# Kernel optimization log

Hardware: AMD Instinct MI355X
Metric: run time of the kernel (lower is better)

The kernel has to match this reference:

```python
import jax, jax.numpy as jnp
import numpy as np

N, H, W = 2048, 128, 128
SH_C0 = 0.28209479177387814
SH_C1 = 0.4886025119029199
_C2 = [1.0925484305920792, -1.0925484305920792, 0.31539156525252005, -1.0925484305920792, 0.5462742152960396]
_C3 = [-0.5900435899266435, 2.890611442640554, -0.4570457994644658, 0.3731763325901154, -0.4570457994644658, 1.445305721320277, -0.5900435899266435]


def _quat_to_rot(q):
    # q: [N,4] unit quaternions (w, x, y, z)
    w, x, y, z = q[:, 0], q[:, 1], q[:, 2], q[:, 3]
    R = jnp.stack([
        1 - 2 * (y * y + z * z), 2 * (x * y - w * z), 2 * (x * z + w * y),
        2 * (x * y + w * z), 1 - 2 * (x * x + z * z), 2 * (y * z - w * x),
        2 * (x * z - w * y), 2 * (y * z + w * x), 1 - 2 * (x * x + y * y)], axis=-1)
    return R.reshape(-1, 3, 3)


def _sh_to_color(sh, dirs):
    # sh: [N,16,3] degree-3 SH coeffs per channel; dirs: [N,3] unit view dirs
    x, y, z = dirs[:, 0:1], dirs[:, 1:2], dirs[:, 2:3]
    xx, yy, zz = x * x, y * y, z * z
    xy, yz, xz = x * y, y * z, x * z
    c = SH_C0 * sh[:, 0]
    c = c - SH_C1 * y * sh[:, 1] + SH_C1 * z * sh[:, 2] - SH_C1 * x * sh[:, 3]
    c = (c + _C2[0] * xy * sh[:, 4] + _C2[1] * yz * sh[:, 5]
         + _C2[2] * (2 * zz - xx - yy) * sh[:, 6] + _C2[3] * xz * sh[:, 7]
         + _C2[4] * (xx - yy) * sh[:, 8])
    c = (c + _C3[0] * y * (3 * xx - yy) * sh[:, 9] + _C3[1] * xy * z * sh[:, 10]
         + _C3[2] * y * (4 * zz - xx - yy) * sh[:, 11]
         + _C3[3] * z * (2 * zz - 3 * xx - 3 * yy) * sh[:, 12]
         + _C3[4] * x * (4 * zz - xx - yy) * sh[:, 13]
         + _C3[5] * z * (xx - yy) * sh[:, 14]
         + _C3[6] * x * (xx - 3 * yy) * sh[:, 15])
    return jnp.maximum(c + 0.5, 0.0)


def _forward(pws, shs, alphas_raw, scales_raw, rots_raw, Rcw, tcw, fx, fy, cx, cy, width, height):
    fx = jnp.float32(fx); fy = jnp.float32(fy)
    cx = jnp.float32(cx); cy = jnp.float32(cy)
    # GSModel activations
    alphas = jax.nn.sigmoid(alphas_raw)[:, 0]                    # [N]
    scales = jnp.exp(scales_raw)                                 # [N,3]
    rots = rots_raw / jnp.linalg.norm(rots_raw, axis=-1, keepdims=True)

    # --- project ---
    pcs = pws @ Rcw.T + tcw                                      # [N,3] camera coords
    depths = pcs[:, 2]
    valid = depths > 0.2                                         # frustum (near-plane) cull
    z = jnp.where(valid, depths, 1.0)
    u = jnp.stack([fx * pcs[:, 0] / z + cx, fy * pcs[:, 1] / z + cy], -1)  # [N,2]

    # --- cov3d = R S S^T R^T ---
    R = _quat_to_rot(rots)
    M = R * scales[:, None, :]                                   # R @ diag(s)
    cov3d = M @ jnp.swapaxes(M, 1, 2)                            # [N,3,3]

    # --- cov2d = T cov3d T^T + lowpass (T = J Rcw, EWA splatting) ---
    limx = 1.3 * 0.5 * width / fx
    limy = 1.3 * 0.5 * height / fy
    tx = jnp.clip(pcs[:, 0] / z, -limx, limx) * z
    ty = jnp.clip(pcs[:, 1] / z, -limy, limy) * z
    zero = jnp.zeros_like(z)
    J = jnp.stack([
        jnp.stack([fx / z, zero, -fx * tx / (z * z)], -1),
        jnp.stack([zero, fy / z, -fy * ty / (z * z)], -1)], 1)   # [N,2,3]
    T = J @ Rcw
    cov2d = T @ cov3d @ jnp.swapaxes(T, 1, 2) + 0.3 * jnp.eye(2, dtype=pws.dtype)

    # --- SH -> color ---
    twc = -Rcw.T @ tcw                                           # camera center in world
    d = pws - twc
    dirs = d / jnp.linalg.norm(d, axis=-1, keepdims=True)
    colors = _sh_to_color(shs.reshape(-1, 16, 3), dirs)          # [N,3]

    # --- inverse cov2d + 3-sigma screen extent (areas) ---
    a, b, c = cov2d[:, 0, 0], cov2d[:, 0, 1], cov2d[:, 1, 1]
    det = a * c - b * b
    valid = valid & (det > 0)
    det_s = jnp.where(valid, det, 1.0)
    cinv = jnp.stack([c / det_s, -b / det_s, a / det_s], -1)     # [N,3] = (c00, c01, c11)
    mid = 0.5 * (a + c)
    disc = jnp.sqrt(jnp.maximum(mid * mid - det, 0.1))
    areas = 3.0 * jnp.sqrt(jnp.maximum(jnp.stack([mid + disc, mid - disc], -1), 0.0))
    areas = jnp.where(valid[:, None], areas, 0.0)                # [N,2]

    # --- depth-sorted alpha compositing (dense reference for tile splat) ---
    order = jnp.argsort(depths)
    u_s, cinv_s = u[order], cinv[order]
    a_s, col_s, v_s = alphas[order], colors[order], valid[order]

    px = jnp.arange(width, dtype=pws.dtype) + 0.5
    py = jnp.arange(height, dtype=pws.dtype) + 0.5
    dx = px[None, None, :] - u_s[:, 0, None, None]               # [N,1,W]
    dy = py[None, :, None] - u_s[:, 1, None, None]               # [N,H,1]
    power = (-0.5 * (cinv_s[:, 0, None, None] * dx * dx
                     + cinv_s[:, 2, None, None] * dy * dy)
             - cinv_s[:, 1, None, None] * dx * dy)               # [N,H,W]
    g = jnp.minimum(a_s[:, None, None] * jnp.exp(jnp.minimum(power, 0.0)), 0.99)
    g = jnp.where((power <= 0.0) & (g >= 1.0 / 255.0) & v_s[:, None, None], g, 0.0)

    tau = jnp.cumprod(1.0 - g, axis=0)                           # transmittance
    T_excl = jnp.concatenate([jnp.ones_like(tau[:1]), tau[:-1]], axis=0)
    image = jnp.einsum('nhw,nc->chw', T_excl * g, col_s)         # [3,H,W]
    return image, areas


def setup_inputs() -> dict:
    key = jax.random.key(0)
    ks = jax.random.split(key, 6)
    pws = jax.random.normal(ks[0], (N, 3), dtype=jnp.float32) * jnp.array([2.0, 2.0, 1.0], jnp.float32)
    pws = pws.at[:, 2].add(5.0)  # in front of camera
    shs = jax.random.normal(ks[1], (N, 48), dtype=jnp.float32) * 0.5
    alphas_raw = jax.random.normal(ks[2], (N, 1), dtype=jnp.float32)
    scales_raw = jax.random.normal(ks[3], (N, 3), dtype=jnp.float32) * 0.3 - 2.0
    rots_raw = jax.random.normal(ks[4], (N, 4), dtype=jnp.float32)
    us = jnp.zeros((N, 2), dtype=jnp.float32)
    Rcw = jnp.eye(3, dtype=jnp.float32)
    tcw = jnp.zeros(3, dtype=jnp.float32)
    return dict(pws=pws, shs=shs, alphas_raw=alphas_raw, scales_raw=scales_raw,
                rots_raw=rots_raw, us=us, Rcw=Rcw, tcw=tcw,
                fx=400, fy=400, cx=64, cy=64, width=W, height=H)


def reference(pws, shs, alphas_raw, scales_raw, rots_raw, us, Rcw, tcw, fx, fy, cx, cy, width, height):
    # 'us' is accepted but recomputed inside (matches gsc.project overwriting it)
    return _forward(pws, shs, alphas_raw, scales_raw, rots_raw, Rcw, tcw, fx, fy, cx, cy, width, height)
```

## Files before the change

kernel.cpp:

```cpp
#include <hip/hip_runtime.h>
#include <hip/hip_fp16.h>
#include <math.h>

#define N_G   2048
#define IMG_W 128
#define IMG_H 128
#define NPIX (IMG_W * IMG_H)

#define RWAVES 16
#define RSUB   (N_G / RWAVES)

union f2h2 { float f; __half2 h; };

__global__ __launch_bounds__(64) void preprocess_k(
    const float* __restrict__ pws, const float* __restrict__ shs,
    const float* __restrict__ alphas_raw, const float* __restrict__ scales_raw,
    const float* __restrict__ rots_raw, const float* __restrict__ Rcw,
    const float* __restrict__ tcw,
    const int* __restrict__ fxp, const int* __restrict__ fyp,
    const int* __restrict__ cxp, const int* __restrict__ cyp,
    float* __restrict__ areas, float* __restrict__ depths,
    float* __restrict__ packed)
{
    int i = blockIdx.x * 64 + threadIdx.x;
    if (i >= N_G) return;

    const float fx = (float)fxp[0], fy = (float)fyp[0];
    const float cx = (float)cxp[0], cy = (float)cyp[0];
    const float R00 = Rcw[0], R01 = Rcw[1], R02 = Rcw[2];
    const float R10 = Rcw[3], R11 = Rcw[4], R12 = Rcw[5];
    const float R20 = Rcw[6], R21 = Rcw[7], R22 = Rcw[8];
    const float t0 = tcw[0], t1 = tcw[1], t2 = tcw[2];

    const float pwx = pws[i * 3 + 0], pwy = pws[i * 3 + 1], pwz = pws[i * 3 + 2];

    const float pcx = R00 * pwx + R01 * pwy + R02 * pwz + t0;
    const float pcy = R10 * pwx + R11 * pwy + R12 * pwz + t1;
    const float pcz = R20 * pwx + R21 * pwy + R22 * pwz + t2;

    const float depth = pcz;
    bool valid = depth > 0.2f;
    const float z = valid ? depth : 1.0f;

    const float ux = fx * pcx / z + cx;
    const float uy = fy * pcy / z + cy;

    const float4 q4 = ((const float4*)rots_raw)[i];
    float qw = q4.x, qx = q4.y, qy = q4.z, qz = q4.w;
    const float qn = sqrtf(qw * qw + qx * qx + qy * qy + qz * qz);
    qw /= qn; qx /= qn; qy /= qn; qz /= qn;
    float Rr[3][3];
    Rr[0][0] = 1.f - 2.f * (qy * qy + qz * qz);
    Rr[0][1] = 2.f * (qx * qy - qw * qz);
    Rr[0][2] = 2.f * (qx * qz + qw * qy);
    Rr[1][0] = 2.f * (qx * qy + qw * qz);
    Rr[1][1] = 1.f - 2.f * (qx * qx + qz * qz);
    Rr[1][2] = 2.f * (qy * qz - qw * qx);
    Rr[2][0] = 2.f * (qx * qz - qw * qy);
    Rr[2][1] = 2.f * (qy * qz + qw * qx);
    Rr[2][2] = 1.f - 2.f * (qx * qx + qy * qy);

    const float s0 = expf(scales_raw[i * 3 + 0]);
    const float s1 = expf(scales_raw[i * 3 + 1]);
    const float s2 = expf(scales_raw[i * 3 + 2]);
    const float sc[3] = { s0, s1, s2 };

    float M[3][3];
    for (int r = 0; r < 3; ++r)
        for (int c = 0; c < 3; ++c) M[r][c] = Rr[r][c] * sc[c];

    float cov[3][3];
    for (int r = 0; r < 3; ++r)
        for (int c = 0; c < 3; ++c)
            cov[r][c] = M[r][0] * M[c][0] + M[r][1] * M[c][1] + M[r][2] * M[c][2];

    const float limx = 1.3f * 0.5f * (float)IMG_W / fx;
    const float limy = 1.3f * 0.5f * (float)IMG_H / fy;
    const float xz_ = pcx / z, yz_ = pcy / z;
    const float tx = fminf(fmaxf(xz_, -limx), limx) * z;
    const float ty = fminf(fmaxf(yz_, -limy), limy) * z;
    const float J00 = fx / z, J02 = -fx * tx / (z * z);
    const float J11 = fy / z, J12 = -fy * ty / (z * z);
    const float T00 = J00 * R00 + J02 * R20;
    const float T01 = J00 * R01 + J02 * R21;
    const float T02 = J00 * R02 + J02 * R22;
    const float T10 = J11 * R10 + J12 * R20;
    const float T11 = J11 * R11 + J12 * R21;
    const float T12 = J11 * R12 + J12 * R22;

    float tmp0[3], tmp1[3];
    for (int k = 0; k < 3; ++k) {
        tmp0[k] = T00 * cov[0][k] + T01 * cov[1][k] + T02 * cov[2][k];
        tmp1[k] = T10 * cov[0][k] + T11 * cov[1][k] + T12 * cov[2][k];
    }
    const float a = tmp0[0] * T00 + tmp0[1] * T01 + tmp0[2] * T02 + 0.3f;
    const float b = tmp0[0] * T10 + tmp0[1] * T11 + tmp0[2] * T12;
    const float c = tmp1[0] * T10 + tmp1[1] * T11 + tmp1[2] * T12 + 0.3f;

    const float twx = -(R00 * t0 + R10 * t1 + R20 * t2);
    const float twy = -(R01 * t0 + R11 * t1 + R21 * t2);
    const float twz = -(R02 * t0 + R12 * t1 + R22 * t2);
    const float ddx = pwx - twx, ddy = pwy - twy, ddz = pwz - twz;
    const float dn = sqrtf(ddx * ddx + ddy * ddy + ddz * ddz);
    const float dirx = ddx / dn, diry = ddy / dn, dirz = ddz / dn;

    const float xx = dirx * dirx, yy = diry * diry, zz = dirz * dirz;
    const float xy = dirx * diry, yz = diry * dirz, xz = dirx * dirz;
    float bf[16];
    bf[0]  = 0.28209479177387814f;
    bf[1]  = -0.4886025119029199f * diry;
    bf[2]  = 0.4886025119029199f * dirz;
    bf[3]  = -0.4886025119029199f * dirx;
    bf[4]  = 1.0925484305920792f * xy;
    bf[5]  = -1.0925484305920792f * yz;
    bf[6]  = 0.31539156525252005f * (2.f * zz - xx - yy);
    bf[7]  = -1.0925484305920792f * xz;
    bf[8]  = 0.5462742152960396f * (xx - yy);
    bf[9]  = -0.5900435899266435f * diry * (3.f * xx - yy);
    bf[10] = 2.890611442640554f * xy * dirz;
    bf[11] = -0.4570457994644658f * diry * (4.f * zz - xx - yy);
    bf[12] = 0.3731763325901154f * dirz * (2.f * zz - 3.f * xx - 3.f * yy);
    bf[13] = -0.4570457994644658f * dirx * (4.f * zz - xx - yy);
    bf[14] = 1.445305721320277f * dirz * (xx - yy);
    bf[15] = -0.5900435899266435f * dirx * (xx - 3.f * yy);

    float sh[48];
    const float4* sh4 = (const float4*)(shs + i * 48);
    #pragma unroll
    for (int k = 0; k < 12; ++k) ((float4*)sh)[k] = sh4[k];

    float col[3];
    for (int ch = 0; ch < 3; ++ch) {
        float acc = 0.f;
        #pragma unroll
        for (int k = 0; k < 16; ++k) acc += bf[k] * sh[k * 3 + ch];
        col[ch] = fmaxf(acc + 0.5f, 0.f);
    }

    const float det = a * c - b * b;
    valid = valid && (det > 0.f);
    const float det_s = valid ? det : 1.0f;
    const float ci0 = c / det_s, ci1 = -b / det_s, ci2 = a / det_s;

    const float mid  = 0.5f * (a + c);
    const float disc = sqrtf(fmaxf(mid * mid - det, 0.1f));
    const float a0 = 3.f * sqrtf(fmaxf(mid + disc, 0.f));
    const float a1 = 3.f * sqrtf(fmaxf(mid - disc, 0.f));
    areas[i * 2 + 0] = valid ? a0 : 0.f;
    areas[i * 2 + 1] = valid ? a1 : 0.f;

    const float alpha = 1.f / (1.f + expf(-alphas_raw[i]));

    depths[i] = depth;

    f2h2 pc; pc.h = __floats2half2_rn(col[0], col[1]);
    float* pk = packed + i * 8;
    pk[0] = ux;  pk[1] = uy;
    pk[2] = -0.5f * ci0; pk[3] = -ci1; pk[4] = -0.5f * ci2;
    pk[5] = valid ? alpha : 0.f;
    pk[6] = pc.f;
    pk[7] = col[2];
}

__global__ __launch_bounds__(512) void rank_scatter_k(
    const float* __restrict__ depths, const float4* __restrict__ packed,
    float4* __restrict__ sorted)
{
    __shared__ float sd[N_G];
    const int tid = threadIdx.x;
    ((float4*)sd)[tid] = ((const float4*)depths)[tid];
    __syncthreads();

    const int w = tid >> 6, lane = tid & 63;
    const int i = blockIdx.x * 8 + w;
    const float d = sd[i];

    int r = 0;
    #pragma unroll 8
    for (int k = 0; k < 32; ++k) {
        const int j = k * 64 + lane;
        const float dj = sd[j];
        const bool c = (dj < d) || (dj == d && j < i);
        r += (int)__popcll(__ballot(c));
    }

    if (lane < 2)
        sorted[r * 2 + lane] = packed[i * 2 + lane];
}

__global__ __launch_bounds__(1024) void raster_k(
    const float4* __restrict__ sorted, float* __restrict__ image)
{
    __shared__ float4 sg[N_G * 2];

    const int tid  = threadIdx.x;
    const int lane = tid & 63;
    const int w    = tid >> 6;

    #pragma unroll
    for (int k = 0; k < 4; ++k)
        sg[tid + k * 1024] = sorted[tid + k * 1024];
    __syncthreads();

    const int p = blockIdx.x * 64 + lane;
    const float px = (float)(p & (IMG_W - 1)) + 0.5f;
    const float py = (float)(p >> 7) + 0.5f;

    float T = 1.f, C0 = 0.f, C1 = 0.f, C2 = 0.f;
    const int base = w * RSUB * 2;
    #pragma unroll 4
    for (int j = 0; j < RSUB; ++j) {
        const float4 r0 = sg[base + j * 2 + 0];
        const float4 r1 = sg[base + j * 2 + 1];
        const float dx = px - r0.x, dy = py - r0.y;
        const float power = r0.z * (dx * dx) + r0.w * (dx * dy) + r1.x * (dy * dy);
        const float e = __expf(fminf(power, 0.f));
        float g = fminf(r1.y * e, 0.99f);
        const bool ok = (power <= 0.f) && (g >= (1.f / 255.f));
        g = ok ? g : 0.f;
        const float wgt = T * g;
        f2h2 cu; cu.f = r1.z;
        C0 += wgt * __low2float(cu.h);
        C1 += wgt * __high2float(cu.h);
        C2 += wgt * r1.w;
        T *= (1.f - g);
    }

    __syncthreads();
    float4* red = sg;
    red[w * 64 + lane] = make_float4(C0, C1, C2, T);
    __syncthreads();

    if (w == 0) {
        float Tacc = 1.f, A0 = 0.f, A1 = 0.f, A2 = 0.f;
        #pragma unroll
        for (int s = 0; s < RWAVES; ++s) {
            const float4 v = red[s * 64 + lane];
            A0 += Tacc * v.x;
            A1 += Tacc * v.y;
            A2 += Tacc * v.z;
            Tacc *= v.w;
        }
        image[p]            = A0;
        image[NPIX + p]     = A1;
        image[2 * NPIX + p] = A2;
    }
}

extern "C" void kernel_launch(void* const* d_in, const int* in_sizes, int n_in,
                              void* d_out, int out_size, void* d_ws, size_t ws_size,
                              hipStream_t stream) {
    const float* pws        = (const float*)d_in[0];
    const float* shs        = (const float*)d_in[1];
    const float* alphas_raw = (const float*)d_in[2];
    const float* scales_raw = (const float*)d_in[3];
    const float* rots_raw   = (const float*)d_in[4];
    const float* Rcw        = (const float*)d_in[6];
    const float* tcw        = (const float*)d_in[7];
    const int*   fxp        = (const int*)d_in[8];
    const int*   fyp        = (const int*)d_in[9];
    const int*   cxp        = (const int*)d_in[10];
    const int*   cyp        = (const int*)d_in[11];

    float* out   = (float*)d_out;
    float* areas = out + 3 * NPIX;

    float* depths = (float*)d_ws;
    float* packed = depths + N_G;
    float* sorted = packed + N_G * 8;

    preprocess_k<<<N_G / 64, 64, 0, stream>>>(
        pws, shs, alphas_raw, scales_raw, rots_raw, Rcw, tcw,
        fxp, fyp, cxp, cyp, areas, depths, packed);

    rank_scatter_k<<<N_G / 8, 512, 0, stream>>>(
        depths, (const float4*)packed, (float4*)sorted);

    raster_k<<<NPIX / 64, 1024, 0, stream>>>((const float4*)sorted, out);
}
```

Measured before the change: 111.1 us.

## Cull gaussians per wavefront row segment with ballot using packed screen radius

Preprocessing now computes a conservative screen-space radius from the larger covariance eigenvalue. It packs that radius as fp16 next to the blue channel and zeroes alpha for gaussians below the 1/255 threshold. The raster kernel tests 64 gaussians at once against the wavefront's 64-pixel row segment, ballots the hits, and evaluates only the hit gaussians, skipping exp and blend work for non-overlapping splats. Blue is now stored at half precision, and the radius-based cull relies on the 3.34*sqrt(lambda) bound covering every contributing pixel.

```diff
diff --git a/kernel.cpp b/kernel.cpp
--- a/kernel.cpp
+++ b/kernel.cpp
@@ -144,22 +144,27 @@
 
     const float mid  = 0.5f * (a + c);
     const float disc = sqrtf(fmaxf(mid * mid - det, 0.1f));
-    const float a0 = 3.f * sqrtf(fmaxf(mid + disc, 0.f));
+    const float lam0 = fmaxf(mid + disc, 0.f);
+    const float a0 = 3.f * sqrtf(lam0);
     const float a1 = 3.f * sqrtf(fmaxf(mid - disc, 0.f));
     areas[i * 2 + 0] = valid ? a0 : 0.f;
     areas[i * 2 + 1] = valid ? a1 : 0.f;
 
     const float alpha = 1.f / (1.f + expf(-alphas_raw[i]));
 
+    const bool vis = valid && (alpha >= (1.f / 255.f));
+    const float rad = vis ? (3.34f * sqrtf(lam0) + 1.0f) : 0.f;
+
     depths[i] = depth;
 
     f2h2 pc; pc.h = __floats2half2_rn(col[0], col[1]);
+    f2h2 cr; cr.h = __floats2half2_rn(col[2], rad);
     float* pk = packed + i * 8;
     pk[0] = ux;  pk[1] = uy;
     pk[2] = -0.5f * ci0; pk[3] = -ci1; pk[4] = -0.5f * ci2;
-    pk[5] = valid ? alpha : 0.f;
+    pk[5] = vis ? alpha : 0.f;
     pk[6] = pc.f;
-    pk[7] = col[2];
+    pk[7] = cr.f;
 }
 
 __global__ __launch_bounds__(512) void rank_scatter_k(
@@ -205,25 +210,44 @@
     const int p = blockIdx.x * 64 + lane;
     const float px = (float)(p & (IMG_W - 1)) + 0.5f;
     const float py = (float)(p >> 7) + 0.5f;
+    const float x0f = (float)((blockIdx.x & 1) * 64) + 0.5f;
+    const float x1f = x0f + 63.0f;
+    const float ycf = py;
 
     float T = 1.f, C0 = 0.f, C1 = 0.f, C2 = 0.f;
-    const int base = w * RSUB * 2;
-    #pragma unroll 4
-    for (int j = 0; j < RSUB; ++j) {
-        const float4 r0 = sg[base + j * 2 + 0];
-        const float4 r1 = sg[base + j * 2 + 1];
-        const float dx = px - r0.x, dy = py - r0.y;
-        const float power = r0.z * (dx * dx) + r0.w * (dx * dy) + r1.x * (dy * dy);
-        const float e = __expf(fminf(power, 0.f));
-        float g = fminf(r1.y * e, 0.99f);
-        const bool ok = (power <= 0.f) && (g >= (1.f / 255.f));
-        g = ok ? g : 0.f;
-        const float wgt = T * g;
-        f2h2 cu; cu.f = r1.z;
-        C0 += wgt * __low2float(cu.h);
-        C1 += wgt * __high2float(cu.h);
-        C2 += wgt * r1.w;
-        T *= (1.f - g);
+
+    #pragma unroll
+    for (int cch = 0; cch < RSUB / 64; ++cch) {
+        const int rbase = w * RSUB + cch * 64;
+        const int rt = rbase + lane;
+        const float tux = sg[rt * 2].x;
+        const float tuy = sg[rt * 2].y;
+        f2h2 tcr; tcr.f = sg[rt * 2 + 1].w;
+        const float trad = __high2float(tcr.h);
+        const bool hit = (fabsf(tuy - ycf) < trad) &&
+                         (tux + trad > x0f) && (tux - trad < x1f);
+        unsigned long long m = __ballot(hit);
+
+        while (m) {
+            const int b = (int)__builtin_ctzll(m);
+            m &= (m - 1);
+            const int rr = rbase + b;
+            const float4 r0 = sg[rr * 2 + 0];
+            const float4 r1 = sg[rr * 2 + 1];
+            const float dx = px - r0.x, dy = py - r0.y;
+            const float power = r0.z * (dx * dx) + r0.w * (dx * dy) + r1.x * (dy * dy);
+            const float e = __expf(fminf(power, 0.f));
+            float g = fminf(r1.y * e, 0.99f);
+            const bool ok = (power <= 0.f) && (g >= (1.f / 255.f));
+            g = ok ? g : 0.f;
+            const float wgt = T * g;
+            f2h2 cu; cu.f = r1.z;
+            f2h2 cv; cv.f = r1.w;
+            C0 += wgt * __low2float(cu.h);
+            C1 += wgt * __high2float(cu.h);
+            C2 += wgt * __low2float(cv.h);
+            T *= (1.f - g);
+        }
     }
 
     __syncthreads();
```

New measurement: 90.91 us. 1.22x faster.
